# Optimization experiments

Hardware: AMD Instinct MI355X
Metric: run time of the kernel (lower is better)

Reference implementation:

```python
import jax, jax.numpy as jnp
import numpy as np

TOPK = 3
IOU_THRESHOLD = 0.5


def setup_inputs() -> dict:
    key = jax.random.key(0)
    k0, k1, k2, k3 = jax.random.split(key, 4)
    S, N, TGT_PER_VID = 256, 128, 4
    M = S * TGT_PER_VID          # 1024 target moments total
    P = N * N                    # 16384 valid proposals (mask2d all ones)
    start_offset = jax.random.normal(k0, (S, P), dtype=jnp.float32) * 0.1
    end_offset = jax.random.normal(k1, (S, P), dtype=jnp.float32) * 0.1
    # target moments: (start, end) in [0,1], start <= end
    tgt_moments = jnp.sort(jax.random.uniform(k2, (M, 2), dtype=jnp.float32), axis=1)
    num_targets = jnp.full((S,), TGT_PER_VID, dtype=jnp.int32)  # sums to M
    iou2ds = jax.random.uniform(k3, (M, N, N), dtype=jnp.float32)
    mask2d = jnp.ones((N, N), dtype=bool)
    return {
        "start_offset": start_offset,
        "end_offset": end_offset,
        "tgt_moments": tgt_moments,
        "num_targets": num_targets,
        "iou2ds": iou2ds,
        "mask2d": mask2d,
    }


def reference(start_offset, end_offset, tgt_moments, num_targets, iou2ds, mask2d):
    M, N, _ = iou2ds.shape
    S, P = start_offset.shape
    # map each of the M targets back to its source video (repeat_interleave)
    scatter_m2s = jnp.repeat(jnp.arange(S), num_targets, total_repeat_length=M)
    so = start_offset[scatter_m2s]  # [M, P]
    eo = end_offset[scatter_m2s]    # [M, P]
    # row-major nonzero positions of mask2d (== torch masked_select ordering)
    rows, cols = jnp.nonzero(mask2d, size=P)
    iou1ds = iou2ds[:, rows, cols]  # [M, P]
    # top-k scatter mask + IoU-threshold mask
    _, topk_idx = jax.lax.top_k(iou1ds, TOPK)  # [M, TOPK]
    target_mask = jnp.zeros((M, P), dtype=start_offset.dtype)
    target_mask = target_mask.at[jnp.arange(M)[:, None], topk_idx].set(1.0)
    target_mask = jnp.where(iou1ds > IOU_THRESHOLD, 1.0, target_mask)
    # scores2ds_to_moments: proposal (row, col) -> moment (row/N, (col+1)/N)
    starts = rows.astype(start_offset.dtype) / N                 # [P]
    ends = (cols.astype(start_offset.dtype) + 1.0) / N           # [P]
    start_offset_target = tgt_moments[:, 0:1] - starts[None, :]  # [M, P]
    end_offset_target = tgt_moments[:, 1:2] - ends[None, :]      # [M, P]
    loss = jnp.abs(so - start_offset_target) + jnp.abs(eo - end_offset_target)
    return (loss * target_mask).sum() / target_mask.sum()
```

## Files before the change

kernel.cpp:

```cpp
#include <hip/hip_runtime.h>
#include <math.h>

#define TOPK_N 3
#define IOU_THR 0.5f
#define NCNT 64
#define THREADS 512
#define NW (THREADS / 64)
#define SENT 0x7fffffff

__device__ __forceinline__ bool better(float va, int ia, float vb, int ib) {
    return (va > vb) || (va == vb && ia < ib);
}

__device__ __forceinline__ void merge3(float& a0, float& a1, float& a2,
                                       int& x0, int& x1, int& x2,
                                       float b0, float b1, float b2,
                                       int y0, int y1, int y2) {
    bool t0 = better(a0, x0, b0, y0);
    float ov0 = t0 ? a0 : b0;  int oi0 = t0 ? x0 : y0;
    float ahv = t0 ? a1 : a0;  int ahi = t0 ? x1 : x0;
    float a2v = t0 ? a2 : a1;  int a2i = t0 ? x2 : x1;
    float bhv = t0 ? b0 : b1;  int bhi = t0 ? y0 : y1;
    float b2v = t0 ? b1 : b2;  int b2i = t0 ? y1 : y2;
    bool t1 = better(ahv, ahi, bhv, bhi);
    float ov1 = t1 ? ahv : bhv; int oi1 = t1 ? ahi : bhi;
    float cav = t1 ? a2v : ahv; int cai = t1 ? a2i : ahi;
    float cbv = t1 ? bhv : b2v; int cbi = t1 ? bhi : b2i;
    bool t2 = better(cav, cai, cbv, cbi);
    a0 = ov0; a1 = ov1; a2 = t2 ? cav : cbv;
    x0 = oi0; x1 = oi1; x2 = t2 ? cai : cbi;
}

__global__ void prep_kernel(const int* __restrict__ num_targets,
                            const int* __restrict__ mask2d,
                            int* __restrict__ scatter,
                            int* __restrict__ counts,
                            int S, int M, int P) {
    const int bid = blockIdx.x;
    const int tid = threadIdx.x;

    if (bid < NCNT) {
        const int P4 = P >> 2;
        const int4* __restrict__ m4 = (const int4*)mask2d;
        int c = 0;
        for (int q = bid * 256 + tid; q < P4; q += NCNT * 256) {
            const int4 v = m4[q];
            c += (v.x != 0) + (v.y != 0) + (v.z != 0) + (v.w != 0);
        }
        if (bid == 0) {
            for (int j = (P4 << 2) + tid; j < P; j += 256)
                c += (mask2d[j] != 0);
        }
        __shared__ int red[256];
        red[tid] = c;
        __syncthreads();
        for (int st = 128; st > 0; st >>= 1) {
            if (tid < st) red[tid] += red[tid + st];
            __syncthreads();
        }
        if (tid == 0) counts[bid] = red[0];
    } else {
        __shared__ int cum[1025];
        __shared__ int scn[256];
        const int chunk = (S + 255) / 256;
        const int sbase = tid * chunk;
        int local[4];
        int csum = 0;
        for (int k = 0; k < chunk && k < 4; ++k) {
            int s = sbase + k;
            int v = (s < S) ? num_targets[s] : 0;
            csum += v;
            local[k] = csum;
        }
        scn[tid] = csum;
        __syncthreads();
        for (int d = 1; d < 256; d <<= 1) {
            int v = scn[tid];
            int add = (tid >= d) ? scn[tid - d] : 0;
            __syncthreads();
            scn[tid] = v + add;
            __syncthreads();
        }
        {
            int excl = scn[tid] - csum;
            for (int k = 0; k < chunk && k < 4; ++k) {
                int s = sbase + k;
                if (s < S) cum[s + 1] = excl + local[k];
            }
            if (tid == 0) cum[0] = 0;
        }
        __syncthreads();
        const int total = cum[S];
        for (int m = tid; m < M; m += 256) {
            int mm = m;
            if (mm >= total) mm = (total > 0) ? (total - 1) : 0;
            int lo = 0, hi = S - 1;
            while (lo < hi) {
                int mid = (lo + hi) >> 1;
                if (cum[mid + 1] <= mm) lo = mid + 1; else hi = mid;
            }
            scatter[m] = lo;
        }
    }
}

__global__ void build_kernel(const int* __restrict__ counts,
                             const int* __restrict__ mask2d,
                             int* __restrict__ rcidx,
                             float* __restrict__ starts,
                             float* __restrict__ ends,
                             int* __restrict__ flag,
                             int N, int P) {
    const int tid = threadIdx.x;
    __shared__ int scan[256];

    scan[tid] = (tid < NCNT) ? counts[tid] : 0;
    __syncthreads();
    for (int st = 128; st > 0; st >>= 1) {
        if (tid < st) scan[tid] += scan[tid + st];
        __syncthreads();
    }
    const int K_all = scan[0];
    const int f = (K_all == P && (P & 3) == 0 && (N & (N - 1)) == 0) ? 1 : 0;
    if (tid == 0) flag[0] = f;
    if (f) return;
    __syncthreads();

    const int per = (P + 255) / 256;
    const int base = tid * per;
    int cnt = 0;
    for (int k = 0; k < per; ++k) {
        int j = base + k;
        if (j < P && mask2d[j] != 0) cnt++;
    }
    scan[tid] = cnt;
    __syncthreads();
    for (int d = 1; d < 256; d <<= 1) {
        int v = scan[tid];
        int add = (tid >= d) ? scan[tid - d] : 0;
        __syncthreads();
        scan[tid] = v + add;
        __syncthreads();
    }
    const int K = scan[255];
    int pos = scan[tid] - cnt;

    const float fN = (float)N;
    for (int k = 0; k < per; ++k) {
        int j = base + k;
        if (j < P && mask2d[j] != 0) {
            int r = j / N;
            int c = j - r * N;
            rcidx[pos]  = j;
            starts[pos] = (float)r / fN;
            ends[pos]   = (float)(c + 1) / fN;
            pos++;
        }
    }
    __syncthreads();
    for (int j = K + tid; j < P; j += 256) {
        rcidx[j]  = 0;
        starts[j] = 0.0f;
        ends[j]   = 1.0f / fN;
    }
}

__global__ __launch_bounds__(THREADS, 8)
void loss_kernel(const float* __restrict__ start_offset,
                 const float* __restrict__ end_offset,
                 const float* __restrict__ tgt_moments,
                 const int* __restrict__ scatter,
                 const float* __restrict__ iou2ds,
                 const int* __restrict__ rcidx,
                 const float* __restrict__ starts,
                 const float* __restrict__ ends,
                 double* __restrict__ psum,
                 int* __restrict__ pcnt,
                 const int* __restrict__ flag,
                 int P, int M, int N) {
    const int bid = blockIdx.x;
    const int m = ((M & 7) == 0) ? ((bid & 7) * (M >> 3) + (bid >> 3)) : bid;
    const int tid = threadIdx.x;
    const int s   = scatter[m];
    const int fp  = flag[0];

    const float* __restrict__ so_row  = start_offset + (size_t)s * P;
    const float* __restrict__ eo_row  = end_offset   + (size_t)s * P;
    const float* __restrict__ iou_row = iou2ds       + (size_t)m * P;
    const float tgt0 = tgt_moments[2 * m];
    const float tgt1 = tgt_moments[2 * m + 1];

    const int   lgN  = 31 - __clz(N);
    const float invN = 1.0f / (float)N;

    float lsum = 0.0f;
    int   lcnt = 0;

    float v0 = -INFINITY, v1 = -INFINITY, v2 = -INFINITY;
    int   i0 = SENT, i1 = SENT, i2 = SENT;

#define PROC(v, jj, so_, eo_, st_, en_)                                     \
    do {                                                                    \
        const bool b0 = (v) > v0;                                           \
        const bool b1 = (v) > v1;                                           \
        const bool b2 = (v) > v2;                                           \
        v2 = b1 ? v1 : (b2 ? (v) : v2);  i2 = b1 ? i1 : (b2 ? (jj) : i2);   \
        v1 = b0 ? v0 : (b1 ? (v) : v1);  i1 = b0 ? i0 : (b1 ? (jj) : i1);   \
        v0 = b0 ? (v) : v0;              i0 = b0 ? (jj) : i0;               \
        const bool sel = (v) > IOU_THR;                                     \
        const float l_ = fabsf((so_) - (tgt0 - (st_))) +                    \
                         fabsf((eo_) - (tgt1 - (en_)));                     \
        lsum += sel ? l_ : 0.0f;                                            \
        lcnt += sel ? 1 : 0;                                                \
    } while (0)

    if (fp) {
        const float4* __restrict__ iou4 = (const float4*)iou_row;
        const float4* __restrict__ so4  = (const float4*)so_row;
        const float4* __restrict__ eo4  = (const float4*)eo_row;
        const int P4 = P >> 2;
        for (int q = tid; q < P4; q += THREADS) {
            const float4 vi = iou4[q];
            const float4 vs = so4[q];
            const float4 ve = eo4[q];
            const int j  = q << 2;
            const int r  = j >> lgN;
            const int c0 = j & (N - 1);
            const float st = (float)r * invN;
            const float e0 = (float)(c0 + 1) * invN;
            const float e1 = (float)(c0 + 2) * invN;
            const float e2 = (float)(c0 + 3) * invN;
            const float e3 = (float)(c0 + 4) * invN;
            PROC(vi.x, j + 0, vs.x, ve.x, st, e0);
            PROC(vi.y, j + 1, vs.y, ve.y, st, e1);
            PROC(vi.z, j + 2, vs.z, ve.z, st, e2);
            PROC(vi.w, j + 3, vs.w, ve.w, st, e3);
        }
    } else {
        for (int j = tid; j < P; j += THREADS) {
            const int   idx = rcidx[j];
            const float v   = iou_row[idx];
            PROC(v, j, so_row[j], eo_row[j], starts[j], ends[j]);
        }
    }
#undef PROC

    for (int d = 1; d < 64; d <<= 1) {
        float bv0 = __shfl_xor(v0, d), bv1 = __shfl_xor(v1, d), bv2 = __shfl_xor(v2, d);
        int   by0 = __shfl_xor(i0, d), by1 = __shfl_xor(i1, d), by2 = __shfl_xor(i2, d);
        merge3(v0, v1, v2, i0, i1, i2, bv0, bv1, bv2, by0, by1, by2);
    }
    double dsum = (double)lsum;
    for (int d = 1; d < 64; d <<= 1) dsum += __shfl_xor(dsum, d);
    for (int d = 1; d < 64; d <<= 1) lcnt += __shfl_xor(lcnt, d);

    __shared__ float  wv[NW][3];
    __shared__ int    wi[NW][3];
    __shared__ double wsum[NW];
    __shared__ int    wcnt[NW];
    const int wid  = tid >> 6;
    const int lane = tid & 63;
    if (lane == 0) {
        wv[wid][0] = v0; wv[wid][1] = v1; wv[wid][2] = v2;
        wi[wid][0] = i0; wi[wid][1] = i1; wi[wid][2] = i2;
        wsum[wid] = dsum; wcnt[wid] = lcnt;
    }
    __syncthreads();

    if (tid == 0) {
        float a0 = wv[0][0], a1 = wv[0][1], a2 = wv[0][2];
        int   x0 = wi[0][0], x1 = wi[0][1], x2 = wi[0][2];
        double S = wsum[0];
        int    C = wcnt[0];
        for (int w = 1; w < NW; ++w) {
            merge3(a0, a1, a2, x0, x1, x2,
                   wv[w][0], wv[w][1], wv[w][2],
                   wi[w][0], wi[w][1], wi[w][2]);
            S += wsum[w];
            C += wcnt[w];
        }
#define ADDTOP(vk, jk)                                                      \
        do {                                                                \
            if ((jk) != SENT && !((vk) > IOU_THR)) {                        \
                float st_, en_;                                             \
                if (fp) {                                                   \
                    int r_ = (jk) >> lgN, c_ = (jk) & (N - 1);              \
                    st_ = (float)r_ * invN; en_ = (float)(c_ + 1) * invN;   \
                } else { st_ = starts[jk]; en_ = ends[jk]; }                \
                S += (double)(fabsf(so_row[jk] - (tgt0 - st_)) +            \
                              fabsf(eo_row[jk] - (tgt1 - en_)));            \
                C += 1;                                                     \
            }                                                               \
        } while (0)
        ADDTOP(a0, x0);
        ADDTOP(a1, x1);
        ADDTOP(a2, x2);
#undef ADDTOP
        psum[bid] = S;
        pcnt[bid] = C;
    }
}

__global__ void finalize_kernel(const double* __restrict__ psum,
                                const int* __restrict__ pcnt,
                                int M, float* __restrict__ out) {
    __shared__ double sd[256];
    __shared__ int    sc[256];
    const int tid = threadIdx.x;
    double a = 0.0;
    int    c = 0;
    for (int i = tid; i < M; i += 256) { a += psum[i]; c += pcnt[i]; }
    sd[tid] = a; sc[tid] = c;
    __syncthreads();
    for (int str = 128; str > 0; str >>= 1) {
        if (tid < str) { sd[tid] += sd[tid + str]; sc[tid] += sc[tid + str]; }
        __syncthreads();
    }
    if (tid == 0) out[0] = (float)(sd[0] / (double)sc[0]);
}

extern "C" void kernel_launch(void* const* d_in, const int* in_sizes, int n_in,
                              void* d_out, int out_size, void* d_ws, size_t ws_size,
                              hipStream_t stream) {
    const float* start_offset = (const float*)d_in[0];
    const float* end_offset   = (const float*)d_in[1];
    const float* tgt_moments  = (const float*)d_in[2];
    const int*   num_targets  = (const int*)d_in[3];
    const float* iou2ds       = (const float*)d_in[4];
    const int*   mask2d       = (const int*)d_in[5];

    const int S = in_sizes[3];
    const int M = in_sizes[2] / 2;
    const int P = in_sizes[0] / S;
    const int NN = in_sizes[5];
    int N = 1;
    while ((long long)N * N < (long long)NN) N++;

    char* ws = (char*)d_ws;
    size_t off = 0;
    int*    flag    = (int*)(ws + off);    off += 16;
    int*    counts  = (int*)(ws + off);    off += (NCNT * 4 + 15) & ~(size_t)15;
    int*    scatter = (int*)(ws + off);    off += ((size_t)M * 4 + 15) & ~(size_t)15;
    int*    rcidx   = (int*)(ws + off);    off += ((size_t)P * 4 + 15) & ~(size_t)15;
    float*  starts  = (float*)(ws + off);  off += ((size_t)P * 4 + 15) & ~(size_t)15;
    float*  ends    = (float*)(ws + off);  off += ((size_t)P * 4 + 15) & ~(size_t)15;
    double* psum    = (double*)(ws + off); off += ((size_t)M * 8 + 15) & ~(size_t)15;
    int*    pcnt    = (int*)(ws + off);    off += ((size_t)M * 4 + 15) & ~(size_t)15;

    prep_kernel<<<NCNT + 1, 256, 0, stream>>>(num_targets, mask2d, scatter, counts,
                                              S, M, P);
    build_kernel<<<1, 256, 0, stream>>>(counts, mask2d, rcidx, starts, ends, flag, N, P);
    loss_kernel<<<M, THREADS, 0, stream>>>(start_offset, end_offset, tgt_moments,
                                           scatter, iou2ds, rcidx, starts, ends,
                                           psum, pcnt, flag, P, M, N);
    finalize_kernel<<<1, 256, 0, stream>>>(psum, pcnt, M, (float*)d_out);
}
```

Baseline: 36.26 us.

## Group targets per video so each block reuses start/end offset rows

A new grouped path runs when every video has exactly four targets. One 1024-thread block then handles all four targets of a video, loading the start/end offset rows once instead of once per target, which cuts redundant global reads. The general per-target path stays as a fallback, and the grid now launches S+M blocks where the unused half exits early. It also uses fmed3/fmax for the top-3 update, reduces the mask-count blocks from 64 to 8, and raises threads per block. Keeping four top-3 states per thread adds register pressure and may lower occupancy.

```diff
diff --git a/kernel.cpp b/kernel.cpp
--- a/kernel.cpp
+++ b/kernel.cpp
@@ -3,9 +3,10 @@
 
 #define TOPK_N 3
 #define IOU_THR 0.5f
-#define NCNT 64
-#define THREADS 512
+#define NCNT 8
+#define THREADS 1024
 #define NW (THREADS / 64)
+#define TPV 4
 #define SENT 0x7fffffff
 
 __device__ __forceinline__ bool better(float va, int ia, float vb, int ib) {
@@ -35,6 +36,7 @@
                             const int* __restrict__ mask2d,
                             int* __restrict__ scatter,
                             int* __restrict__ counts,
+                            int* __restrict__ uniform_flag,
                             int S, int M, int P) {
     const int bid = blockIdx.x;
     const int tid = threadIdx.x;
@@ -62,23 +64,31 @@
     } else {
         __shared__ int cum[1025];
         __shared__ int scn[256];
+        __shared__ int uni[256];
         const int chunk = (S + 255) / 256;
         const int sbase = tid * chunk;
         int local[4];
         int csum = 0;
+        int ok = 1;
         for (int k = 0; k < chunk && k < 4; ++k) {
             int s = sbase + k;
-            int v = (s < S) ? num_targets[s] : 0;
-            csum += v;
+            int v = (s < S) ? num_targets[s] : TPV;
+            if (s < S && v != TPV) ok = 0;
+            csum += (s < S) ? v : 0;
             local[k] = csum;
         }
         scn[tid] = csum;
+        uni[tid] = ok;
         __syncthreads();
         for (int d = 1; d < 256; d <<= 1) {
             int v = scn[tid];
             int add = (tid >= d) ? scn[tid - d] : 0;
             __syncthreads();
             scn[tid] = v + add;
+            __syncthreads();
+        }
+        for (int st = 128; st > 0; st >>= 1) {
+            if (tid < st) uni[tid] &= uni[tid + st];
             __syncthreads();
         }
         {
@@ -91,6 +101,8 @@
         }
         __syncthreads();
         const int total = cum[S];
+        if (tid == 0)
+            uniform_flag[0] = (uni[0] && total == M && M == TPV * S) ? 1 : 0;
         for (int m = tid; m < M; m += 256) {
             int mm = m;
             if (mm >= total) mm = (total > 0) ? (total - 1) : 0;
@@ -121,7 +133,7 @@
         __syncthreads();
     }
     const int K_all = scan[0];
-    const int f = (K_all == P && (P & 3) == 0 && (N & (N - 1)) == 0) ? 1 : 0;
+    const int f = (K_all == P && (P & 3) == 0 && (N & (N - 1)) == 0 && N >= 4) ? 1 : 0;
     if (tid == 0) flag[0] = f;
     if (f) return;
     __syncthreads();
@@ -165,7 +177,7 @@
     }
 }
 
-__global__ __launch_bounds__(THREADS, 8)
+__global__ __launch_bounds__(THREADS, 4)
 void loss_kernel(const float* __restrict__ start_offset,
                  const float* __restrict__ end_offset,
                  const float* __restrict__ tgt_moments,
@@ -177,43 +189,187 @@
                  double* __restrict__ psum,
                  int* __restrict__ pcnt,
                  const int* __restrict__ flag,
-                 int P, int M, int N) {
+                 const int* __restrict__ uniform_flag,
+                 int P, int M, int N, int S) {
     const int bid = blockIdx.x;
-    const int m = ((M & 7) == 0) ? ((bid & 7) * (M >> 3) + (bid >> 3)) : bid;
     const int tid = threadIdx.x;
-    const int s   = scatter[m];
     const int fp  = flag[0];
-
+    const int grouped = fp && uniform_flag[0];
+
+    const int   lgN  = 31 - __clz(N);
+    const float invN = 1.0f / (float)N;
+
+#define PROC(ST, v, jj, so_, eo_, A_, B_)                                   \
+    do {                                                                    \
+        const bool b0 = (v) > v0##ST;                                       \
+        const bool b1 = (v) > v1##ST;                                       \
+        const bool b2 = (v) > v2##ST;                                       \
+        const float nv0 = fmaxf(v0##ST, (v));                               \
+        const float nv1 = __builtin_amdgcn_fmed3f((v), v0##ST, v1##ST);     \
+        const float nv2 = __builtin_amdgcn_fmed3f((v), v1##ST, v2##ST);     \
+        i2##ST = b1 ? i1##ST : (b2 ? (jj) : i2##ST);                        \
+        i1##ST = b0 ? i0##ST : (b1 ? (jj) : i1##ST);                        \
+        i0##ST = b0 ? (jj) : i0##ST;                                        \
+        v0##ST = nv0; v1##ST = nv1; v2##ST = nv2;                           \
+        const bool sel = (v) > IOU_THR;                                     \
+        const float l_ = fabsf((so_) - (A_)) + fabsf((eo_) - (B_));         \
+        ls##ST += sel ? l_ : 0.0f;                                          \
+        lc##ST += sel ? 1 : 0;                                              \
+    } while (0)
+
+    if (bid < S) {
+        if (!grouped) return;
+        const int s  = bid;
+        const int m0 = s * TPV;
+        const float* __restrict__ so_row = start_offset + (size_t)s * P;
+        const float* __restrict__ eo_row = end_offset   + (size_t)s * P;
+        const float4* __restrict__ so4 = (const float4*)so_row;
+        const float4* __restrict__ eo4 = (const float4*)eo_row;
+        const float4* __restrict__ io0 = (const float4*)(iou2ds + (size_t)(m0 + 0) * P);
+        const float4* __restrict__ io1 = (const float4*)(iou2ds + (size_t)(m0 + 1) * P);
+        const float4* __restrict__ io2 = (const float4*)(iou2ds + (size_t)(m0 + 2) * P);
+        const float4* __restrict__ io3 = (const float4*)(iou2ds + (size_t)(m0 + 3) * P);
+        const float t0_0 = tgt_moments[2 * m0 + 0], t1_0 = tgt_moments[2 * m0 + 1];
+        const float t0_1 = tgt_moments[2 * m0 + 2], t1_1 = tgt_moments[2 * m0 + 3];
+        const float t0_2 = tgt_moments[2 * m0 + 4], t1_2 = tgt_moments[2 * m0 + 5];
+        const float t0_3 = tgt_moments[2 * m0 + 6], t1_3 = tgt_moments[2 * m0 + 7];
+
+        float v0_0 = -INFINITY, v1_0 = -INFINITY, v2_0 = -INFINITY;
+        float v0_1 = -INFINITY, v1_1 = -INFINITY, v2_1 = -INFINITY;
+        float v0_2 = -INFINITY, v1_2 = -INFINITY, v2_2 = -INFINITY;
+        float v0_3 = -INFINITY, v1_3 = -INFINITY, v2_3 = -INFINITY;
+        int i0_0 = SENT, i1_0 = SENT, i2_0 = SENT;
+        int i0_1 = SENT, i1_1 = SENT, i2_1 = SENT;
+        int i0_2 = SENT, i1_2 = SENT, i2_2 = SENT;
+        int i0_3 = SENT, i1_3 = SENT, i2_3 = SENT;
+        float ls_0 = 0.f, ls_1 = 0.f, ls_2 = 0.f, ls_3 = 0.f;
+        int   lc_0 = 0,   lc_1 = 0,   lc_2 = 0,   lc_3 = 0;
+
+#define PROCM(ST, vi, t0_, t1_)                                             \
+    do {                                                                    \
+        const float A_ = (t0_) - stv;                                       \
+        PROC(ST, (vi).x, j_ + 0, vs.x, ve.x, A_, (t1_) - en0);              \
+        PROC(ST, (vi).y, j_ + 1, vs.y, ve.y, A_, (t1_) - en1);              \
+        PROC(ST, (vi).z, j_ + 2, vs.z, ve.z, A_, (t1_) - en2);              \
+        PROC(ST, (vi).w, j_ + 3, vs.w, ve.w, A_, (t1_) - en3);              \
+    } while (0)
+
+        const int P4 = P >> 2;
+        for (int q = tid; q < P4; q += THREADS) {
+            const float4 vs  = so4[q];
+            const float4 ve  = eo4[q];
+            const float4 vi0 = io0[q];
+            const float4 vi1 = io1[q];
+            const float4 vi2 = io2[q];
+            const float4 vi3 = io3[q];
+            const int j_ = q << 2;
+            const int r_ = j_ >> lgN;
+            const int c_ = j_ & (N - 1);
+            const float stv = (float)r_ * invN;
+            const float en0 = (float)(c_ + 1) * invN;
+            const float en1 = en0 + invN;
+            const float en2 = en0 + 2.0f * invN;
+            const float en3 = en0 + 3.0f * invN;
+            PROCM(_0, vi0, t0_0, t1_0);
+            PROCM(_1, vi1, t0_1, t1_1);
+            PROCM(_2, vi2, t0_2, t1_2);
+            PROCM(_3, vi3, t0_3, t1_3);
+        }
+#undef PROCM
+
+#define WREDUCE(ST)                                                         \
+        for (int d = 1; d < 64; d <<= 1) {                                  \
+            float b0v = __shfl_xor(v0##ST, d), b1v = __shfl_xor(v1##ST, d), \
+                  b2v = __shfl_xor(v2##ST, d);                              \
+            int   y0 = __shfl_xor(i0##ST, d), y1 = __shfl_xor(i1##ST, d),   \
+                  y2 = __shfl_xor(i2##ST, d);                               \
+            merge3(v0##ST, v1##ST, v2##ST, i0##ST, i1##ST, i2##ST,          \
+                   b0v, b1v, b2v, y0, y1, y2);                              \
+        }
+        WREDUCE(_0) WREDUCE(_1) WREDUCE(_2) WREDUCE(_3)
+#undef WREDUCE
+        double ds_0 = (double)ls_0, ds_1 = (double)ls_1;
+        double ds_2 = (double)ls_2, ds_3 = (double)ls_3;
+        for (int d = 1; d < 64; d <<= 1) {
+            ds_0 += __shfl_xor(ds_0, d); ds_1 += __shfl_xor(ds_1, d);
+            ds_2 += __shfl_xor(ds_2, d); ds_3 += __shfl_xor(ds_3, d);
+            lc_0 += __shfl_xor(lc_0, d); lc_1 += __shfl_xor(lc_1, d);
+            lc_2 += __shfl_xor(lc_2, d); lc_3 += __shfl_xor(lc_3, d);
+        }
+
+        __shared__ float  gwv[NW][TPV][3];
+        __shared__ int    gwi[NW][TPV][3];
+        __shared__ double gws[NW][TPV];
+        __shared__ int    gwc[NW][TPV];
+        const int wid  = tid >> 6;
+        const int lane = tid & 63;
+        if (lane == 0) {
+            gwv[wid][0][0] = v0_0; gwv[wid][0][1] = v1_0; gwv[wid][0][2] = v2_0;
+            gwv[wid][1][0] = v0_1; gwv[wid][1][1] = v1_1; gwv[wid][1][2] = v2_1;
+            gwv[wid][2][0] = v0_2; gwv[wid][2][1] = v1_2; gwv[wid][2][2] = v2_2;
+            gwv[wid][3][0] = v0_3; gwv[wid][3][1] = v1_3; gwv[wid][3][2] = v2_3;
+            gwi[wid][0][0] = i0_0; gwi[wid][0][1] = i1_0; gwi[wid][0][2] = i2_0;
+            gwi[wid][1][0] = i0_1; gwi[wid][1][1] = i1_1; gwi[wid][1][2] = i2_1;
+            gwi[wid][2][0] = i0_2; gwi[wid][2][1] = i1_2; gwi[wid][2][2] = i2_2;
+            gwi[wid][3][0] = i0_3; gwi[wid][3][1] = i1_3; gwi[wid][3][2] = i2_3;
+            gws[wid][0] = ds_0; gws[wid][1] = ds_1;
+            gws[wid][2] = ds_2; gws[wid][3] = ds_3;
+            gwc[wid][0] = lc_0; gwc[wid][1] = lc_1;
+            gwc[wid][2] = lc_2; gwc[wid][3] = lc_3;
+        }
+        __syncthreads();
+
+        if (tid < TPV) {
+            const int km = tid;
+            const float t0m = tgt_moments[2 * (m0 + km) + 0];
+            const float t1m = tgt_moments[2 * (m0 + km) + 1];
+            float a0 = gwv[0][km][0], a1 = gwv[0][km][1], a2 = gwv[0][km][2];
+            int   x0 = gwi[0][km][0], x1 = gwi[0][km][1], x2 = gwi[0][km][2];
+            double Ssum = gws[0][km];
+            int    C    = gwc[0][km];
+            for (int w = 1; w < NW; ++w) {
+                merge3(a0, a1, a2, x0, x1, x2,
+                       gwv[w][km][0], gwv[w][km][1], gwv[w][km][2],
+                       gwi[w][km][0], gwi[w][km][1], gwi[w][km][2]);
+                Ssum += gws[w][km];
+                C    += gwc[w][km];
+            }
+#define ADDTOPG(vk, jk)                                                     \
+            do {                                                            \
+                if ((jk) != SENT && !((vk) > IOU_THR)) {                    \
+                    int r_ = (jk) >> lgN, c_ = (jk) & (N - 1);              \
+                    float st_ = (float)r_ * invN;                           \
+                    float en_ = (float)(c_ + 1) * invN;                     \
+                    Ssum += (double)(fabsf(so_row[jk] - (t0m - st_)) +      \
+                                     fabsf(eo_row[jk] - (t1m - en_)));      \
+                    C += 1;                                                 \
+                }                                                           \
+            } while (0)
+            ADDTOPG(a0, x0);
+            ADDTOPG(a1, x1);
+            ADDTOPG(a2, x2);
+#undef ADDTOPG
+            psum[m0 + km] = Ssum;
+            pcnt[m0 + km] = C;
+        }
+        return;
+    }
+
+    if (grouped) return;
+    const int m = bid - S;
+    if (m >= M) return;
+    const int s = scatter[m];
     const float* __restrict__ so_row  = start_offset + (size_t)s * P;
     const float* __restrict__ eo_row  = end_offset   + (size_t)s * P;
     const float* __restrict__ iou_row = iou2ds       + (size_t)m * P;
     const float tgt0 = tgt_moments[2 * m];
     const float tgt1 = tgt_moments[2 * m + 1];
 
-    const int   lgN  = 31 - __clz(N);
-    const float invN = 1.0f / (float)N;
-
-    float lsum = 0.0f;
-    int   lcnt = 0;
-
-    float v0 = -INFINITY, v1 = -INFINITY, v2 = -INFINITY;
-    int   i0 = SENT, i1 = SENT, i2 = SENT;
-
-#define PROC(v, jj, so_, eo_, st_, en_)                                     \
-    do {                                                                    \
-        const bool b0 = (v) > v0;                                           \
-        const bool b1 = (v) > v1;                                           \
-        const bool b2 = (v) > v2;                                           \
-        v2 = b1 ? v1 : (b2 ? (v) : v2);  i2 = b1 ? i1 : (b2 ? (jj) : i2);   \
-        v1 = b0 ? v0 : (b1 ? (v) : v1);  i1 = b0 ? i0 : (b1 ? (jj) : i1);   \
-        v0 = b0 ? (v) : v0;              i0 = b0 ? (jj) : i0;               \
-        const bool sel = (v) > IOU_THR;                                     \
-        const float l_ = fabsf((so_) - (tgt0 - (st_))) +                    \
-                         fabsf((eo_) - (tgt1 - (en_)));                     \
-        lsum += sel ? l_ : 0.0f;                                            \
-        lcnt += sel ? 1 : 0;                                                \
-    } while (0)
-
+    float v0_f = -INFINITY, v1_f = -INFINITY, v2_f = -INFINITY;
+    int   i0_f = SENT, i1_f = SENT, i2_f = SENT;
+    float ls_f = 0.0f;
+    int   lc_f = 0;
+#define v0_F v0_f
     if (fp) {
         const float4* __restrict__ iou4 = (const float4*)iou_row;
         const float4* __restrict__ so4  = (const float4*)so_row;
@@ -223,36 +379,36 @@
             const float4 vi = iou4[q];
             const float4 vs = so4[q];
             const float4 ve = eo4[q];
-            const int j  = q << 2;
-            const int r  = j >> lgN;
-            const int c0 = j & (N - 1);
-            const float st = (float)r * invN;
-            const float e0 = (float)(c0 + 1) * invN;
-            const float e1 = (float)(c0 + 2) * invN;
-            const float e2 = (float)(c0 + 3) * invN;
-            const float e3 = (float)(c0 + 4) * invN;
-            PROC(vi.x, j + 0, vs.x, ve.x, st, e0);
-            PROC(vi.y, j + 1, vs.y, ve.y, st, e1);
-            PROC(vi.z, j + 2, vs.z, ve.z, st, e2);
-            PROC(vi.w, j + 3, vs.w, ve.w, st, e3);
+            const int j_ = q << 2;
+            const int r_ = j_ >> lgN;
+            const int c_ = j_ & (N - 1);
+            const float A_  = tgt0 - (float)r_ * invN;
+            const float en0 = (float)(c_ + 1) * invN;
+            PROC(_f, vi.x, j_ + 0, vs.x, ve.x, A_, tgt1 - en0);
+            PROC(_f, vi.y, j_ + 1, vs.y, ve.y, A_, tgt1 - (en0 + invN));
+            PROC(_f, vi.z, j_ + 2, vs.z, ve.z, A_, tgt1 - (en0 + 2.0f * invN));
+            PROC(_f, vi.w, j_ + 3, vs.w, ve.w, A_, tgt1 - (en0 + 3.0f * invN));
         }
     } else {
         for (int j = tid; j < P; j += THREADS) {
             const int   idx = rcidx[j];
             const float v   = iou_row[idx];
-            PROC(v, j, so_row[j], eo_row[j], starts[j], ends[j]);
-        }
-    }
+            const float A_  = tgt0 - starts[j];
+            const float B_  = tgt1 - ends[j];
+            PROC(_f, v, j, so_row[j], eo_row[j], A_, B_);
+        }
+    }
+#undef v0_F
 #undef PROC
 
     for (int d = 1; d < 64; d <<= 1) {
-        float bv0 = __shfl_xor(v0, d), bv1 = __shfl_xor(v1, d), bv2 = __shfl_xor(v2, d);
-        int   by0 = __shfl_xor(i0, d), by1 = __shfl_xor(i1, d), by2 = __shfl_xor(i2, d);
-        merge3(v0, v1, v2, i0, i1, i2, bv0, bv1, bv2, by0, by1, by2);
-    }
-    double dsum = (double)lsum;
+        float b0v = __shfl_xor(v0_f, d), b1v = __shfl_xor(v1_f, d), b2v = __shfl_xor(v2_f, d);
+        int   y0 = __shfl_xor(i0_f, d), y1 = __shfl_xor(i1_f, d), y2 = __shfl_xor(i2_f, d);
+        merge3(v0_f, v1_f, v2_f, i0_f, i1_f, i2_f, b0v, b1v, b2v, y0, y1, y2);
+    }
+    double dsum = (double)ls_f;
     for (int d = 1; d < 64; d <<= 1) dsum += __shfl_xor(dsum, d);
-    for (int d = 1; d < 64; d <<= 1) lcnt += __shfl_xor(lcnt, d);
+    for (int d = 1; d < 64; d <<= 1) lc_f += __shfl_xor(lc_f, d);
 
     __shared__ float  wv[NW][3];
     __shared__ int    wi[NW][3];
@@ -261,23 +417,23 @@
     const int wid  = tid >> 6;
     const int lane = tid & 63;
     if (lane == 0) {
-        wv[wid][0] = v0; wv[wid][1] = v1; wv[wid][2] = v2;
-        wi[wid][0] = i0; wi[wid][1] = i1; wi[wid][2] = i2;
-        wsum[wid] = dsum; wcnt[wid] = lcnt;
+        wv[wid][0] = v0_f; wv[wid][1] = v1_f; wv[wid][2] = v2_f;
+        wi[wid][0] = i0_f; wi[wid][1] = i1_f; wi[wid][2] = i2_f;
+        wsum[wid] = dsum; wcnt[wid] = lc_f;
     }
     __syncthreads();
 
     if (tid == 0) {
         float a0 = wv[0][0], a1 = wv[0][1], a2 = wv[0][2];
         int   x0 = wi[0][0], x1 = wi[0][1], x2 = wi[0][2];
-        double S = wsum[0];
-        int    C = wcnt[0];
+        double Ssum = wsum[0];
+        int    C    = wcnt[0];
         for (int w = 1; w < NW; ++w) {
             merge3(a0, a1, a2, x0, x1, x2,
                    wv[w][0], wv[w][1], wv[w][2],
                    wi[w][0], wi[w][1], wi[w][2]);
-            S += wsum[w];
-            C += wcnt[w];
+            Ssum += wsum[w];
+            C    += wcnt[w];
         }
 #define ADDTOP(vk, jk)                                                      \
         do {                                                                \
@@ -287,8 +443,8 @@
                     int r_ = (jk) >> lgN, c_ = (jk) & (N - 1);              \
                     st_ = (float)r_ * invN; en_ = (float)(c_ + 1) * invN;   \
                 } else { st_ = starts[jk]; en_ = ends[jk]; }                \
-                S += (double)(fabsf(so_row[jk] - (tgt0 - st_)) +            \
-                              fabsf(eo_row[jk] - (tgt1 - en_)));            \
+                Ssum += (double)(fabsf(so_row[jk] - (tgt0 - st_)) +         \
+                                 fabsf(eo_row[jk] - (tgt1 - en_)));         \
                 C += 1;                                                     \
             }                                                               \
         } while (0)
@@ -296,8 +452,8 @@
         ADDTOP(a1, x1);
         ADDTOP(a2, x2);
 #undef ADDTOP
-        psum[bid] = S;
-        pcnt[bid] = C;
+        psum[m] = Ssum;
+        pcnt[m] = C;
     }
 }
 
@@ -338,20 +494,21 @@
 
     char* ws = (char*)d_ws;
     size_t off = 0;
-    int*    flag    = (int*)(ws + off);    off += 16;
-    int*    counts  = (int*)(ws + off);    off += (NCNT * 4 + 15) & ~(size_t)15;
-    int*    scatter = (int*)(ws + off);    off += ((size_t)M * 4 + 15) & ~(size_t)15;
-    int*    rcidx   = (int*)(ws + off);    off += ((size_t)P * 4 + 15) & ~(size_t)15;
-    float*  starts  = (float*)(ws + off);  off += ((size_t)P * 4 + 15) & ~(size_t)15;
-    float*  ends    = (float*)(ws + off);  off += ((size_t)P * 4 + 15) & ~(size_t)15;
-    double* psum    = (double*)(ws + off); off += ((size_t)M * 8 + 15) & ~(size_t)15;
-    int*    pcnt    = (int*)(ws + off);    off += ((size_t)M * 4 + 15) & ~(size_t)15;
+    int*    flag     = (int*)(ws + off);    off += 16;
+    int*    uflag    = (int*)(ws + off);    off += 16;
+    int*    counts   = (int*)(ws + off);    off += (NCNT * 4 + 15) & ~(size_t)15;
+    int*    scatter  = (int*)(ws + off);    off += ((size_t)M * 4 + 15) & ~(size_t)15;
+    int*    rcidx    = (int*)(ws + off);    off += ((size_t)P * 4 + 15) & ~(size_t)15;
+    float*  starts   = (float*)(ws + off);  off += ((size_t)P * 4 + 15) & ~(size_t)15;
+    float*  ends     = (float*)(ws + off);  off += ((size_t)P * 4 + 15) & ~(size_t)15;
+    double* psum     = (double*)(ws + off); off += ((size_t)M * 8 + 15) & ~(size_t)15;
+    int*    pcnt     = (int*)(ws + off);    off += ((size_t)M * 4 + 15) & ~(size_t)15;
 
     prep_kernel<<<NCNT + 1, 256, 0, stream>>>(num_targets, mask2d, scatter, counts,
-                                              S, M, P);
+                                              uflag, S, M, P);
     build_kernel<<<1, 256, 0, stream>>>(counts, mask2d, rcidx, starts, ends, flag, N, P);
-    loss_kernel<<<M, THREADS, 0, stream>>>(start_offset, end_offset, tgt_moments,
-                                           scatter, iou2ds, rcidx, starts, ends,
-                                           psum, pcnt, flag, P, M, N);
+    loss_kernel<<<S + M, THREADS, 0, stream>>>(start_offset, end_offset, tgt_moments,
+                                               scatter, iou2ds, rcidx, starts, ends,
+                                               psum, pcnt, flag, uflag, P, M, N, S);
     finalize_kernel<<<1, 256, 0, stream>>>(psum, pcnt, M, (float*)d_out);
 }
```

New measurement: 44.67 us. 1.23x slower.

## Pair targets sharing a video per block, split proposals across slices, fuse finalize

Applied to the files above, without the earlier changes.

The loss kernel now has each block process two targets from the same video, so one load of the start/end offset rows serves two IoU rows. This path is taken only when every video has exactly four targets. The proposal range is split into slices across more, smaller 256-thread blocks. Per-slice top-3 candidates and partial sums go to workspace, and a single 1024-thread kernel merges them and applies the top-k correction, replacing the old finalize. The top-3 insertion uses fmax/med3, which cuts selects, at the cost of an extra merge stage and a larger workspace.

```diff
diff --git a/kernel.cpp b/kernel.cpp
--- a/kernel.cpp
+++ b/kernel.cpp
@@ -1,11 +1,11 @@
 #include <hip/hip_runtime.h>
 #include <math.h>
 
-#define TOPK_N 3
 #define IOU_THR 0.5f
-#define NCNT 64
-#define THREADS 512
-#define NW (THREADS / 64)
+#define NCNT 8
+#define FS 8
+#define GS 2
+#define TPV 4
 #define SENT 0x7fffffff
 
 __device__ __forceinline__ bool better(float va, int ia, float vb, int ib) {
@@ -35,6 +35,7 @@
                             const int* __restrict__ mask2d,
                             int* __restrict__ scatter,
                             int* __restrict__ counts,
+                            int* __restrict__ uniform_flag,
                             int S, int M, int P) {
     const int bid = blockIdx.x;
     const int tid = threadIdx.x;
@@ -62,23 +63,31 @@
     } else {
         __shared__ int cum[1025];
         __shared__ int scn[256];
+        __shared__ int uni[256];
         const int chunk = (S + 255) / 256;
         const int sbase = tid * chunk;
         int local[4];
         int csum = 0;
+        int ok = 1;
         for (int k = 0; k < chunk && k < 4; ++k) {
             int s = sbase + k;
-            int v = (s < S) ? num_targets[s] : 0;
-            csum += v;
+            int v = (s < S) ? num_targets[s] : TPV;
+            if (s < S && v != TPV) ok = 0;
+            csum += (s < S) ? v : 0;
             local[k] = csum;
         }
         scn[tid] = csum;
+        uni[tid] = ok;
         __syncthreads();
         for (int d = 1; d < 256; d <<= 1) {
             int v = scn[tid];
             int add = (tid >= d) ? scn[tid - d] : 0;
             __syncthreads();
             scn[tid] = v + add;
+            __syncthreads();
+        }
+        for (int st = 128; st > 0; st >>= 1) {
+            if (tid < st) uni[tid] &= uni[tid + st];
             __syncthreads();
         }
         {
@@ -91,6 +100,8 @@
         }
         __syncthreads();
         const int total = cum[S];
+        if (tid == 0)
+            uniform_flag[0] = (uni[0] && total == M && M == TPV * S) ? 1 : 0;
         for (int m = tid; m < M; m += 256) {
             int mm = m;
             if (mm >= total) mm = (total > 0) ? (total - 1) : 0;
@@ -121,7 +132,7 @@
         __syncthreads();
     }
     const int K_all = scan[0];
-    const int f = (K_all == P && (P & 3) == 0 && (N & (N - 1)) == 0) ? 1 : 0;
+    const int f = (K_all == P && (P & 3) == 0 && (N & (N - 1)) == 0 && N >= 4) ? 1 : 0;
     if (tid == 0) flag[0] = f;
     if (f) return;
     __syncthreads();
@@ -165,7 +176,7 @@
     }
 }
 
-__global__ __launch_bounds__(THREADS, 8)
+__global__ __launch_bounds__(256, 4)
 void loss_kernel(const float* __restrict__ start_offset,
                  const float* __restrict__ end_offset,
                  const float* __restrict__ tgt_moments,
@@ -174,111 +185,295 @@
                  const int* __restrict__ rcidx,
                  const float* __restrict__ starts,
                  const float* __restrict__ ends,
-                 double* __restrict__ psum,
-                 int* __restrict__ pcnt,
+                 float* __restrict__ opv, int* __restrict__ opi,
+                 double* __restrict__ ops, int* __restrict__ opc,
                  const int* __restrict__ flag,
+                 const int* __restrict__ uflag,
                  int P, int M, int N) {
-    const int bid = blockIdx.x;
-    const int m = ((M & 7) == 0) ? ((bid & 7) * (M >> 3) + (bid >> 3)) : bid;
+    const int blk = blockIdx.x;
     const int tid = threadIdx.x;
-    const int s   = scatter[m];
     const int fp  = flag[0];
-
+    const int P4  = P >> 2;
+    const bool grouped = fp && uflag[0] && ((M & 1) == 0) &&
+                         (P4 % (GS * 256 * 4) == 0);
+    const int   lgN  = 31 - __clz(N);
+    const float invN = 1.0f / (float)N;
+
+#define PROC(ST, v, jj, so_, eo_, A_, B_)                                   \
+    do {                                                                    \
+        const bool b0 = (v) > v0##ST;                                       \
+        const bool b1 = (v) > v1##ST;                                       \
+        const bool b2 = (v) > v2##ST;                                       \
+        const float nv0 = fmaxf(v0##ST, (v));                               \
+        const float nv1 = __builtin_amdgcn_fmed3f((v), v0##ST, v1##ST);     \
+        const float nv2 = __builtin_amdgcn_fmed3f((v), v1##ST, v2##ST);     \
+        i2##ST = b1 ? i1##ST : (b2 ? (jj) : i2##ST);                        \
+        i1##ST = b0 ? i0##ST : (b1 ? (jj) : i1##ST);                        \
+        i0##ST = b0 ? (jj) : i0##ST;                                        \
+        v0##ST = nv0; v1##ST = nv1; v2##ST = nv2;                           \
+        const bool sel = (v) > IOU_THR;                                     \
+        const float l_ = fabsf((so_) - (A_)) + fabsf((eo_) - (B_));         \
+        ls##ST += sel ? l_ : 0.0f;                                          \
+        lc##ST += sel ? 1 : 0;                                              \
+    } while (0)
+
+    if (grouped) {
+        if (blk >= M) return;
+        int m0, half;
+        const int HM = M >> 1;
+        if ((HM & 7) == 0 && (M & 3) == 0) {
+            const int g = blk % HM, dup = blk / HM;
+            m0 = ((g >> 1) << 2) + (dup << 1);
+            half = g & 1;
+        } else {
+            m0 = blk & ~1;
+            half = blk & 1;
+        }
+        const int m1 = m0 + 1;
+        const int s  = scatter[m0];
+
+        const float4* __restrict__ so4 = (const float4*)(start_offset + (size_t)s * P);
+        const float4* __restrict__ eo4 = (const float4*)(end_offset   + (size_t)s * P);
+        const float4* __restrict__ ioA = (const float4*)(iou2ds + (size_t)m0 * P);
+        const float4* __restrict__ ioB = (const float4*)(iou2ds + (size_t)m1 * P);
+        const float t00 = tgt_moments[2 * m0],     t10 = tgt_moments[2 * m0 + 1];
+        const float t01 = tgt_moments[2 * m1],     t11 = tgt_moments[2 * m1 + 1];
+
+        float v0_0 = -INFINITY, v1_0 = -INFINITY, v2_0 = -INFINITY;
+        int   i0_0 = SENT, i1_0 = SENT, i2_0 = SENT;
+        float ls_0 = 0.f; int lc_0 = 0;
+        float v0_1 = -INFINITY, v1_1 = -INFINITY, v2_1 = -INFINITY;
+        int   i0_1 = SENT, i1_1 = SENT, i2_1 = SENT;
+        float ls_1 = 0.f; int lc_1 = 0;
+
+#define GELEM(q_, VS, VE, VA, VB)                                           \
+    do {                                                                    \
+        const int j_ = (q_) << 2;                                           \
+        const int r_ = j_ >> lgN;                                           \
+        const int c_ = j_ & (N - 1);                                        \
+        const float stv = (float)r_ * invN;                                 \
+        const float en0 = (float)(c_ + 1) * invN;                           \
+        const float en1 = en0 + invN;                                       \
+        const float en2 = en0 + 2.0f * invN;                                \
+        const float en3 = en0 + 3.0f * invN;                                \
+        const float A0_ = t00 - stv, A1_ = t01 - stv;                       \
+        PROC(_0, (VA).x, j_ + 0, (VS).x, (VE).x, A0_, t10 - en0);           \
+        PROC(_0, (VA).y, j_ + 1, (VS).y, (VE).y, A0_, t10 - en1);           \
+        PROC(_0, (VA).z, j_ + 2, (VS).z, (VE).z, A0_, t10 - en2);           \
+        PROC(_0, (VA).w, j_ + 3, (VS).w, (VE).w, A0_, t10 - en3);           \
+        PROC(_1, (VB).x, j_ + 0, (VS).x, (VE).x, A1_, t11 - en0);           \
+        PROC(_1, (VB).y, j_ + 1, (VS).y, (VE).y, A1_, t11 - en1);           \
+        PROC(_1, (VB).z, j_ + 2, (VS).z, (VE).z, A1_, t11 - en2);           \
+        PROC(_1, (VB).w, j_ + 3, (VS).w, (VE).w, A1_, t11 - en3);           \
+    } while (0)
+
+        const int qlen  = P4 / GS;
+        const int q0    = half * qlen;
+        const int iters = qlen >> 8;
+        for (int b = 0; b < iters; b += 4) {
+            const int qq = q0 + b * 256 + tid;
+            const float4 sA = so4[qq],       sB = so4[qq + 256],
+                         sC = so4[qq + 512], sD = so4[qq + 768];
+            const float4 eA = eo4[qq],       eB = eo4[qq + 256],
+                         eC = eo4[qq + 512], eD = eo4[qq + 768];
+            const float4 aA = ioA[qq],       aB = ioA[qq + 256],
+                         aC = ioA[qq + 512], aD = ioA[qq + 768];
+            const float4 bA = ioB[qq],       bB = ioB[qq + 256],
+                         bC = ioB[qq + 512], bD = ioB[qq + 768];
+            GELEM(qq,       sA, eA, aA, bA);
+            GELEM(qq + 256, sB, eB, aB, bB);
+            GELEM(qq + 512, sC, eC, aC, bC);
+            GELEM(qq + 768, sD, eD, aD, bD);
+        }
+#undef GELEM
+
+        for (int d = 1; d < 64; d <<= 1) {
+            float b0v = __shfl_xor(v0_0, d), b1v = __shfl_xor(v1_0, d), b2v = __shfl_xor(v2_0, d);
+            int   y0 = __shfl_xor(i0_0, d), y1 = __shfl_xor(i1_0, d), y2 = __shfl_xor(i2_0, d);
+            merge3(v0_0, v1_0, v2_0, i0_0, i1_0, i2_0, b0v, b1v, b2v, y0, y1, y2);
+        }
+        for (int d = 1; d < 64; d <<= 1) {
+            float b0v = __shfl_xor(v0_1, d), b1v = __shfl_xor(v1_1, d), b2v = __shfl_xor(v2_1, d);
+            int   y0 = __shfl_xor(i0_1, d), y1 = __shfl_xor(i1_1, d), y2 = __shfl_xor(i2_1, d);
+            merge3(v0_1, v1_1, v2_1, i0_1, i1_1, i2_1, b0v, b1v, b2v, y0, y1, y2);
+        }
+        double ds0 = (double)ls_0, ds1 = (double)ls_1;
+        for (int d = 1; d < 64; d <<= 1) {
+            ds0 += __shfl_xor(ds0, d); ds1 += __shfl_xor(ds1, d);
+            lc_0 += __shfl_xor(lc_0, d); lc_1 += __shfl_xor(lc_1, d);
+        }
+
+        __shared__ float  wv[4][2][3];
+        __shared__ int    wi[4][2][3];
+        __shared__ double wsm[4][2];
+        __shared__ int    wct[4][2];
+        const int wid  = tid >> 6;
+        const int lane = tid & 63;
+        if (lane == 0) {
+            wv[wid][0][0] = v0_0; wv[wid][0][1] = v1_0; wv[wid][0][2] = v2_0;
+            wv[wid][1][0] = v0_1; wv[wid][1][1] = v1_1; wv[wid][1][2] = v2_1;
+            wi[wid][0][0] = i0_0; wi[wid][0][1] = i1_0; wi[wid][0][2] = i2_0;
+            wi[wid][1][0] = i0_1; wi[wid][1][1] = i1_1; wi[wid][1][2] = i2_1;
+            wsm[wid][0] = ds0; wsm[wid][1] = ds1;
+            wct[wid][0] = lc_0; wct[wid][1] = lc_1;
+        }
+        __syncthreads();
+        if (tid < 2) {
+            const int km = tid;
+            float a0 = wv[0][km][0], a1 = wv[0][km][1], a2 = wv[0][km][2];
+            int   x0 = wi[0][km][0], x1 = wi[0][km][1], x2 = wi[0][km][2];
+            double Sm = wsm[0][km];
+            int    Cm = wct[0][km];
+            for (int w = 1; w < 4; ++w) {
+                merge3(a0, a1, a2, x0, x1, x2,
+                       wv[w][km][0], wv[w][km][1], wv[w][km][2],
+                       wi[w][km][0], wi[w][km][1], wi[w][km][2]);
+                Sm += wsm[w][km];
+                Cm += wct[w][km];
+            }
+            const int slot = (km == 0 ? m0 : m1) * FS + half;
+            opv[slot * 3 + 0] = a0; opv[slot * 3 + 1] = a1; opv[slot * 3 + 2] = a2;
+            opi[slot * 3 + 0] = x0; opi[slot * 3 + 1] = x1; opi[slot * 3 + 2] = x2;
+            ops[slot] = Sm;
+            opc[slot] = Cm;
+        }
+        return;
+    }
+
+    const int m  = blk >> 3;
+    const int sl = blk & (FS - 1);
+    if (m >= M) return;
+    const int s = scatter[m];
     const float* __restrict__ so_row  = start_offset + (size_t)s * P;
     const float* __restrict__ eo_row  = end_offset   + (size_t)s * P;
     const float* __restrict__ iou_row = iou2ds       + (size_t)m * P;
     const float tgt0 = tgt_moments[2 * m];
     const float tgt1 = tgt_moments[2 * m + 1];
 
-    const int   lgN  = 31 - __clz(N);
-    const float invN = 1.0f / (float)N;
-
-    float lsum = 0.0f;
-    int   lcnt = 0;
-
-    float v0 = -INFINITY, v1 = -INFINITY, v2 = -INFINITY;
-    int   i0 = SENT, i1 = SENT, i2 = SENT;
-
-#define PROC(v, jj, so_, eo_, st_, en_)                                     \
-    do {                                                                    \
-        const bool b0 = (v) > v0;                                           \
-        const bool b1 = (v) > v1;                                           \
-        const bool b2 = (v) > v2;                                           \
-        v2 = b1 ? v1 : (b2 ? (v) : v2);  i2 = b1 ? i1 : (b2 ? (jj) : i2);   \
-        v1 = b0 ? v0 : (b1 ? (v) : v1);  i1 = b0 ? i0 : (b1 ? (jj) : i1);   \
-        v0 = b0 ? (v) : v0;              i0 = b0 ? (jj) : i0;               \
-        const bool sel = (v) > IOU_THR;                                     \
-        const float l_ = fabsf((so_) - (tgt0 - (st_))) +                    \
-                         fabsf((eo_) - (tgt1 - (en_)));                     \
-        lsum += sel ? l_ : 0.0f;                                            \
-        lcnt += sel ? 1 : 0;                                                \
-    } while (0)
+    float v0_0 = -INFINITY, v1_0 = -INFINITY, v2_0 = -INFINITY;
+    int   i0_0 = SENT, i1_0 = SENT, i2_0 = SENT;
+    float ls_0 = 0.0f; int lc_0 = 0;
 
     if (fp) {
         const float4* __restrict__ iou4 = (const float4*)iou_row;
         const float4* __restrict__ so4  = (const float4*)so_row;
         const float4* __restrict__ eo4  = (const float4*)eo_row;
-        const int P4 = P >> 2;
-        for (int q = tid; q < P4; q += THREADS) {
+        const int q4len = (P4 + FS - 1) / FS;
+        const int q0 = sl * q4len;
+        const int qe = min(q0 + q4len, P4);
+        for (int q = q0 + tid; q < qe; q += 256) {
             const float4 vi = iou4[q];
             const float4 vs = so4[q];
             const float4 ve = eo4[q];
-            const int j  = q << 2;
-            const int r  = j >> lgN;
-            const int c0 = j & (N - 1);
-            const float st = (float)r * invN;
-            const float e0 = (float)(c0 + 1) * invN;
-            const float e1 = (float)(c0 + 2) * invN;
-            const float e2 = (float)(c0 + 3) * invN;
-            const float e3 = (float)(c0 + 4) * invN;
-            PROC(vi.x, j + 0, vs.x, ve.x, st, e0);
-            PROC(vi.y, j + 1, vs.y, ve.y, st, e1);
-            PROC(vi.z, j + 2, vs.z, ve.z, st, e2);
-            PROC(vi.w, j + 3, vs.w, ve.w, st, e3);
+            const int j_ = q << 2;
+            const int r_ = j_ >> lgN;
+            const int c_ = j_ & (N - 1);
+            const float A_  = tgt0 - (float)r_ * invN;
+            const float en0 = (float)(c_ + 1) * invN;
+            PROC(_0, vi.x, j_ + 0, vs.x, ve.x, A_, tgt1 - en0);
+            PROC(_0, vi.y, j_ + 1, vs.y, ve.y, A_, tgt1 - (en0 + invN));
+            PROC(_0, vi.z, j_ + 2, vs.z, ve.z, A_, tgt1 - (en0 + 2.0f * invN));
+            PROC(_0, vi.w, j_ + 3, vs.w, ve.w, A_, tgt1 - (en0 + 3.0f * invN));
         }
     } else {
-        for (int j = tid; j < P; j += THREADS) {
+        const int plen = (P + FS - 1) / FS;
+        const int j0 = sl * plen;
+        const int je = min(j0 + plen, P);
+        for (int j = j0 + tid; j < je; j += 256) {
             const int   idx = rcidx[j];
             const float v   = iou_row[idx];
-            PROC(v, j, so_row[j], eo_row[j], starts[j], ends[j]);
+            const float A_  = tgt0 - starts[j];
+            const float B_  = tgt1 - ends[j];
+            PROC(_0, v, j, so_row[j], eo_row[j], A_, B_);
         }
     }
 #undef PROC
 
     for (int d = 1; d < 64; d <<= 1) {
-        float bv0 = __shfl_xor(v0, d), bv1 = __shfl_xor(v1, d), bv2 = __shfl_xor(v2, d);
-        int   by0 = __shfl_xor(i0, d), by1 = __shfl_xor(i1, d), by2 = __shfl_xor(i2, d);
-        merge3(v0, v1, v2, i0, i1, i2, bv0, bv1, bv2, by0, by1, by2);
-    }
-    double dsum = (double)lsum;
+        float b0v = __shfl_xor(v0_0, d), b1v = __shfl_xor(v1_0, d), b2v = __shfl_xor(v2_0, d);
+        int   y0 = __shfl_xor(i0_0, d), y1 = __shfl_xor(i1_0, d), y2 = __shfl_xor(i2_0, d);
+        merge3(v0_0, v1_0, v2_0, i0_0, i1_0, i2_0, b0v, b1v, b2v, y0, y1, y2);
+    }
+    double dsum = (double)ls_0;
     for (int d = 1; d < 64; d <<= 1) dsum += __shfl_xor(dsum, d);
-    for (int d = 1; d < 64; d <<= 1) lcnt += __shfl_xor(lcnt, d);
-
-    __shared__ float  wv[NW][3];
-    __shared__ int    wi[NW][3];
-    __shared__ double wsum[NW];
-    __shared__ int    wcnt[NW];
+    for (int d = 1; d < 64; d <<= 1) lc_0 += __shfl_xor(lc_0, d);
+
+    __shared__ float  fwv[4][3];
+    __shared__ int    fwi[4][3];
+    __shared__ double fws[4];
+    __shared__ int    fwc[4];
     const int wid  = tid >> 6;
     const int lane = tid & 63;
     if (lane == 0) {
-        wv[wid][0] = v0; wv[wid][1] = v1; wv[wid][2] = v2;
-        wi[wid][0] = i0; wi[wid][1] = i1; wi[wid][2] = i2;
-        wsum[wid] = dsum; wcnt[wid] = lcnt;
+        fwv[wid][0] = v0_0; fwv[wid][1] = v1_0; fwv[wid][2] = v2_0;
+        fwi[wid][0] = i0_0; fwi[wid][1] = i1_0; fwi[wid][2] = i2_0;
+        fws[wid] = dsum; fwc[wid] = lc_0;
     }
     __syncthreads();
-
     if (tid == 0) {
-        float a0 = wv[0][0], a1 = wv[0][1], a2 = wv[0][2];
-        int   x0 = wi[0][0], x1 = wi[0][1], x2 = wi[0][2];
-        double S = wsum[0];
-        int    C = wcnt[0];
-        for (int w = 1; w < NW; ++w) {
+        float a0 = fwv[0][0], a1 = fwv[0][1], a2 = fwv[0][2];
+        int   x0 = fwi[0][0], x1 = fwi[0][1], x2 = fwi[0][2];
+        double Sm = fws[0];
+        int    Cm = fwc[0];
+        for (int w = 1; w < 4; ++w) {
             merge3(a0, a1, a2, x0, x1, x2,
-                   wv[w][0], wv[w][1], wv[w][2],
-                   wi[w][0], wi[w][1], wi[w][2]);
-            S += wsum[w];
-            C += wcnt[w];
-        }
+                   fwv[w][0], fwv[w][1], fwv[w][2],
+                   fwi[w][0], fwi[w][1], fwi[w][2]);
+            Sm += fws[w];
+            Cm += fwc[w];
+        }
+        const int slot = m * FS + sl;
+        opv[slot * 3 + 0] = a0; opv[slot * 3 + 1] = a1; opv[slot * 3 + 2] = a2;
+        opi[slot * 3 + 0] = x0; opi[slot * 3 + 1] = x1; opi[slot * 3 + 2] = x2;
+        ops[slot] = Sm;
+        opc[slot] = Cm;
+    }
+}
+
+__global__ void merge_finalize_kernel(const float* __restrict__ opv,
+                                      const int* __restrict__ opi,
+                                      const double* __restrict__ ops,
+                                      const int* __restrict__ opc,
+                                      const float* __restrict__ start_offset,
+                                      const float* __restrict__ end_offset,
+                                      const float* __restrict__ tgt_moments,
+                                      const int* __restrict__ scatter,
+                                      const float* __restrict__ starts,
+                                      const float* __restrict__ ends,
+                                      const int* __restrict__ flag,
+                                      const int* __restrict__ uflag,
+                                      float* __restrict__ out,
+                                      int P, int M, int N) {
+    const int tid = threadIdx.x;
+    const int fp  = flag[0];
+    const int P4  = P >> 2;
+    const bool grouped = fp && uflag[0] && ((M & 1) == 0) &&
+                         (P4 % (GS * 256 * 4) == 0);
+    const int slices = grouped ? GS : FS;
+    const int   lgN  = 31 - __clz(N);
+    const float invN = 1.0f / (float)N;
+
+    double S = 0.0;
+    int    C = 0;
+    for (int m = tid; m < M; m += 1024) {
+        const int base = m * FS;
+        float a0 = opv[base * 3 + 0], a1 = opv[base * 3 + 1], a2 = opv[base * 3 + 2];
+        int   x0 = opi[base * 3 + 0], x1 = opi[base * 3 + 1], x2 = opi[base * 3 + 2];
+        double Sm = ops[base];
+        int    Cm = opc[base];
+        for (int sl = 1; sl < slices; ++sl) {
+            const int b = base + sl;
+            merge3(a0, a1, a2, x0, x1, x2,
+                   opv[b * 3 + 0], opv[b * 3 + 1], opv[b * 3 + 2],
+                   opi[b * 3 + 0], opi[b * 3 + 1], opi[b * 3 + 2]);
+            Sm += ops[b];
+            Cm += opc[b];
+        }
+        const int s = scatter[m];
+        const float* __restrict__ so_row = start_offset + (size_t)s * P;
+        const float* __restrict__ eo_row = end_offset   + (size_t)s * P;
+        const float tgt0 = tgt_moments[2 * m];
+        const float tgt1 = tgt_moments[2 * m + 1];
 #define ADDTOP(vk, jk)                                                      \
         do {                                                                \
             if ((jk) != SENT && !((vk) > IOU_THR)) {                        \
@@ -287,36 +482,35 @@
                     int r_ = (jk) >> lgN, c_ = (jk) & (N - 1);              \
                     st_ = (float)r_ * invN; en_ = (float)(c_ + 1) * invN;   \
                 } else { st_ = starts[jk]; en_ = ends[jk]; }                \
-                S += (double)(fabsf(so_row[jk] - (tgt0 - st_)) +            \
-                              fabsf(eo_row[jk] - (tgt1 - en_)));            \
-                C += 1;                                                     \
+                Sm += (double)(fabsf(so_row[jk] - (tgt0 - st_)) +           \
+                               fabsf(eo_row[jk] - (tgt1 - en_)));           \
+                Cm += 1;                                                    \
             }                                                               \
         } while (0)
         ADDTOP(a0, x0);
         ADDTOP(a1, x1);
         ADDTOP(a2, x2);
 #undef ADDTOP
-        psum[bid] = S;
-        pcnt[bid] = C;
-    }
-}
-
-__global__ void finalize_kernel(const double* __restrict__ psum,
-                                const int* __restrict__ pcnt,
-                                int M, float* __restrict__ out) {
-    __shared__ double sd[256];
-    __shared__ int    sc[256];
-    const int tid = threadIdx.x;
-    double a = 0.0;
-    int    c = 0;
-    for (int i = tid; i < M; i += 256) { a += psum[i]; c += pcnt[i]; }
-    sd[tid] = a; sc[tid] = c;
+        S += Sm;
+        C += Cm;
+    }
+
+    for (int d = 1; d < 64; d <<= 1) {
+        S += __shfl_xor(S, d);
+        C += __shfl_xor(C, d);
+    }
+    __shared__ double sd[16];
+    __shared__ int    sc[16];
+    const int wid  = tid >> 6;
+    const int lane = tid & 63;
+    if (lane == 0) { sd[wid] = S; sc[wid] = C; }
     __syncthreads();
-    for (int str = 128; str > 0; str >>= 1) {
-        if (tid < str) { sd[tid] += sd[tid + str]; sc[tid] += sc[tid + str]; }
-        __syncthreads();
-    }
-    if (tid == 0) out[0] = (float)(sd[0] / (double)sc[0]);
+    if (tid == 0) {
+        double T = 0.0;
+        int    Ct = 0;
+        for (int w = 0; w < 16; ++w) { T += sd[w]; Ct += sc[w]; }
+        out[0] = (float)(T / (double)Ct);
+    }
 }
 
 extern "C" void kernel_launch(void* const* d_in, const int* in_sizes, int n_in,
@@ -338,20 +532,27 @@
 
     char* ws = (char*)d_ws;
     size_t off = 0;
+    const size_t MB = (size_t)M * FS;
     int*    flag    = (int*)(ws + off);    off += 16;
+    int*    uflag   = (int*)(ws + off);    off += 16;
     int*    counts  = (int*)(ws + off);    off += (NCNT * 4 + 15) & ~(size_t)15;
     int*    scatter = (int*)(ws + off);    off += ((size_t)M * 4 + 15) & ~(size_t)15;
     int*    rcidx   = (int*)(ws + off);    off += ((size_t)P * 4 + 15) & ~(size_t)15;
     float*  starts  = (float*)(ws + off);  off += ((size_t)P * 4 + 15) & ~(size_t)15;
     float*  ends    = (float*)(ws + off);  off += ((size_t)P * 4 + 15) & ~(size_t)15;
-    double* psum    = (double*)(ws + off); off += ((size_t)M * 8 + 15) & ~(size_t)15;
-    int*    pcnt    = (int*)(ws + off);    off += ((size_t)M * 4 + 15) & ~(size_t)15;
+    float*  opv     = (float*)(ws + off);  off += (MB * 12 + 15) & ~(size_t)15;
+    int*    opi     = (int*)(ws + off);    off += (MB * 12 + 15) & ~(size_t)15;
+    double* ops     = (double*)(ws + off); off += (MB * 8 + 15) & ~(size_t)15;
+    int*    opc     = (int*)(ws + off);    off += (MB * 4 + 15) & ~(size_t)15;
 
     prep_kernel<<<NCNT + 1, 256, 0, stream>>>(num_targets, mask2d, scatter, counts,
-                                              S, M, P);
+                                              uflag, S, M, P);
     build_kernel<<<1, 256, 0, stream>>>(counts, mask2d, rcidx, starts, ends, flag, N, P);
-    loss_kernel<<<M, THREADS, 0, stream>>>(start_offset, end_offset, tgt_moments,
-                                           scatter, iou2ds, rcidx, starts, ends,
-                                           psum, pcnt, flag, P, M, N);
-    finalize_kernel<<<1, 256, 0, stream>>>(psum, pcnt, M, (float*)d_out);
-}
+    loss_kernel<<<M * FS, 256, 0, stream>>>(start_offset, end_offset, tgt_moments,
+                                            scatter, iou2ds, rcidx, starts, ends,
+                                            opv, opi, ops, opc, flag, uflag, P, M, N);
+    merge_finalize_kernel<<<1, 1024, 0, stream>>>(opv, opi, ops, opc,
+                                                  start_offset, end_offset, tgt_moments,
+                                                  scatter, starts, ends, flag, uflag,
+                                                  (float*)d_out, P, M, N);
+}
```

Result: slower. 42.61 us (+17.5%).
